# Optimization experiments

Measured on AMD Instinct MI355X. Metric: run time of the kernel, lower is better.

The kernel has to match this reference:

```python
import jax, jax.numpy as jnp
import numpy as np

N_ITERS = 5
STRICT_MAXIMA_BONUS = 10.0
MAX_SUBPIXEL_SHIFT = 0.6
DILATION_RADIUS = 1
EPS = 1e-7


def _dense_solve(x):
    """Per-voxel 3x3x3 quadratic-fit solve (Cramer's rule) on interior voxels.

    Returns full-size (zero-padded) sx, sy, ss, g.s, solved arrays.
    Axis convention: s = depth/scale (D), y = height (H), x = width (W).
    """
    c  = x[:, :, 1:-1, 1:-1, 1:-1]
    xp = x[:, :, 1:-1, 1:-1, 2:];   xm = x[:, :, 1:-1, 1:-1, :-2]
    yp = x[:, :, 1:-1, 2:, 1:-1];   ym = x[:, :, 1:-1, :-2, 1:-1]
    sp = x[:, :, 2:, 1:-1, 1:-1];   sm = x[:, :, :-2, 1:-1, 1:-1]
    xpyp = x[:, :, 1:-1, 2:, 2:];   xmyp = x[:, :, 1:-1, 2:, :-2]
    xpym = x[:, :, 1:-1, :-2, 2:];  xmym = x[:, :, 1:-1, :-2, :-2]
    xpsp = x[:, :, 2:, 1:-1, 2:];   xmsp = x[:, :, 2:, 1:-1, :-2]
    xpsm = x[:, :, :-2, 1:-1, 2:];  xmsm = x[:, :, :-2, 1:-1, :-2]
    ypsp = x[:, :, 2:, 2:, 1:-1];   ymsp = x[:, :, 2:, :-2, 1:-1]
    ypsm = x[:, :, :-2, 2:, 1:-1];  ymsm = x[:, :, :-2, :-2, 1:-1]
    gx = 0.5 * (xp - xm)
    gy = 0.5 * (yp - ym)
    gs = 0.5 * (sp - sm)
    dxx = xp - 2.0 * c + xm
    dyy = yp - 2.0 * c + ym
    dss = sp - 2.0 * c + sm
    dxy = 0.25 * (xpyp - xmyp - xpym + xmym)
    dxs = 0.25 * (xpsp - xmsp - xpsm + xmsm)
    dys = 0.25 * (ypsp - ymsp - ypsm + ymsm)
    cf00 = dyy * dss - dys * dys
    cf01 = dxy * dss - dys * dxs
    cf02 = dxy * dys - dyy * dxs
    det = dxx * cf00 - dxy * cf01 + dxs * cf02
    solved = jnp.abs(det) > EPS
    safe_det = jnp.where(solved, det, jnp.ones_like(det))
    r0, r1, r2 = -gx, -gy, -gs
    sx = (r0 * cf00 - dxy * (r1 * dss - dys * r2) + dxs * (r1 * dys - dyy * r2)) / safe_det
    sy = (dxx * (r1 * dss - dys * r2) - r0 * cf01 + dxs * (dxy * r2 - r1 * dxs)) / safe_det
    ss = (dxx * (dyy * r2 - r1 * dys) - dxy * (dxy * r2 - r1 * dxs) + r0 * cf02) / safe_det
    gds = gx * sx + gy * sy + gs * ss
    pad = ((0, 0), (0, 0), (1, 1), (1, 1), (1, 1))
    return (jnp.pad(sx, pad), jnp.pad(sy, pad), jnp.pad(ss, pad),
            jnp.pad(gds, pad), jnp.pad(solved, pad))


def reference(input, nms_mask):
    x = input
    B, C, D, H, W = x.shape
    dt = x.dtype
    HW = H * W
    DHW = D * HW
    r = DILATION_RADIUS

    sx_f, sy_f, ss_f, gds_f, sol_f = _dense_solve(x)
    sx_f = sx_f.reshape(-1); sy_f = sy_f.reshape(-1); ss_f = ss_f.reshape(-1)
    gds_f = gds_f.reshape(-1); sol_f = sol_f.reshape(-1)
    xf = x.reshape(-1)

    dg = jnp.arange(D, dtype=jnp.int32)[:, None, None]
    hg = jnp.arange(H, dtype=jnp.int32)[None, :, None]
    wg = jnp.arange(W, dtype=jnp.int32)[None, None, :]
    bcg = (jnp.arange(B * C, dtype=jnp.int32) * DHW).reshape(B, C, 1, 1, 1)

    zi = jnp.zeros((B, C, D, H, W), jnp.int32)
    dd, dh, dw = zi, zi, zi              # integer centre offsets (s, y, x)
    valid = nms_mask                      # only NMS maxima are tracked
    zf = jnp.zeros((B, C, D, H, W), dt)
    shift_x, shift_y, shift_s, gds_k = zf, zf, zf, zf

    for _ in range(N_ITERS):
        di = jnp.clip(dg + dd, 1, D - 2)
        hi = jnp.clip(hg + dh, 1, H - 2)
        wi = jnp.clip(wg + dw, 1, W - 2)
        flat = bcg + di * HW + hi * W + wi
        sx = sx_f[flat]; sy = sy_f[flat]; ss = ss_f[flat]
        gds = gds_f[flat]; sol = sol_f[flat]
        valid = valid & sol
        vf = valid.astype(dt)
        shift_x = sx * vf
        shift_y = sy * vf
        shift_s = ss * vf
        gds_k = gds * vf
        step_x = (jnp.sign(shift_x) * (jnp.abs(shift_x) > MAX_SUBPIXEL_SHIFT)).astype(jnp.int32)
        step_y = (jnp.sign(shift_y) * (jnp.abs(shift_y) > MAX_SUBPIXEL_SHIFT)).astype(jnp.int32)
        step_s = (jnp.sign(shift_s) * (jnp.abs(shift_s) > MAX_SUBPIXEL_SHIFT)).astype(jnp.int32)
        dw = dw + step_x; dh = dh + step_y; dd = dd + step_s
        # moving outside the dilated precompute region invalidates the keypoint
        valid = valid & (jnp.abs(dd) <= r) & (jnp.abs(dh) <= r) & (jnp.abs(dw) <= r)

    di = jnp.clip(dg + dd, 1, D - 2)
    hi = jnp.clip(hg + dh, 1, H - 2)
    wi = jnp.clip(wg + dw, 1, W - 2)
    flat = bcg + di * HW + hi * W + wi
    cur_val = xf[flat]

    refined = jnp.where(valid, cur_val + 0.5 * gds_k, x)
    y_max = jnp.where(nms_mask, refined + STRICT_MAXIMA_BONUS, x)

    fd = dg.astype(dt); fh = hg.astype(dt); fw = wg.astype(dt)
    cs = jnp.where(valid, (dg + dd).astype(dt) + shift_s, jnp.broadcast_to(fd, x.shape))
    cx = jnp.where(valid, (wg + dw).astype(dt) + shift_x, jnp.broadcast_to(fw, x.shape))
    cy = jnp.where(valid, (hg + dh).astype(dt) + shift_y, jnp.broadcast_to(fh, x.shape))
    coords_max = jnp.stack([cs, cx, cy], axis=2)  # (B,C,3,D,H,W): [scale, x, y]
    return coords_max, y_max


def setup_inputs() -> dict:
    key = jax.random.key(0)
    k1, k2 = jax.random.split(key)
    B, C, D, H, W = 2, 4, 6, 512, 512
    x = jax.random.normal(k1, (B, C, D, H, W), dtype=jnp.float32)
    m = jax.random.uniform(k2, (B, C, D, H, W)) < 0.001
    interior = jnp.zeros((B, C, D, H, W), dtype=bool).at[:, :, 1:-1, 1:-1, 1:-1].set(True)
    return {"input": x, "nms_mask": m & interior}
```

## Files before the change

kernel.cpp:

```cpp
#include <hip/hip_runtime.h>

#pragma clang fp contract(off)

constexpr int B_ = 2, C_ = 4, D_ = 6, H_ = 512, W_ = 512;
constexpr int HW_  = H_ * W_;
constexpr int DHW_ = D_ * HW_;
constexpr int BC_  = B_ * C_;
constexpr int TOT_ = BC_ * DHW_;

#define EPS_ 1e-7f
#define MAX_SHIFT_ 0.6f
#define BONUS_ 10.0f
#define N_ITERS_ 5

__device__ __forceinline__ void solve3(const float* __restrict__ p,
                                       float& sx, float& sy, float& ss,
                                       float& gds, bool& sol)
{
    #pragma clang fp contract(off)
    float c    = p[0];
    float xp   = p[1],          xm   = p[-1];
    float yp   = p[W_],         ym   = p[-W_];
    float spv  = p[HW_],        smv  = p[-HW_];
    float xpyp = p[W_ + 1],     xmyp = p[W_ - 1];
    float xpym = p[-W_ + 1],    xmym = p[-W_ - 1];
    float xpsp = p[HW_ + 1],    xmsp = p[HW_ - 1];
    float xpsm = p[-HW_ + 1],   xmsm = p[-HW_ - 1];
    float ypsp = p[HW_ + W_],   ymsp = p[HW_ - W_];
    float ypsm = p[-HW_ + W_],  ymsm = p[-HW_ - W_];

    float gx = 0.5f * (xp - xm);
    float gy = 0.5f * (yp - ym);
    float gs = 0.5f * (spv - smv);
    float dxx = xp - 2.0f * c + xm;
    float dyy = yp - 2.0f * c + ym;
    float dss = spv - 2.0f * c + smv;
    float dxy = 0.25f * (xpyp - xmyp - xpym + xmym);
    float dxs = 0.25f * (xpsp - xmsp - xpsm + xmsm);
    float dys = 0.25f * (ypsp - ymsp - ypsm + ymsm);

    float cf00 = dyy * dss - dys * dys;
    float cf01 = dxy * dss - dys * dxs;
    float cf02 = dxy * dys - dyy * dxs;
    float det  = dxx * cf00 - dxy * cf01 + dxs * cf02;
    sol = fabsf(det) > EPS_;
    float sd = sol ? det : 1.0f;
    float r0 = -gx, r1 = -gy, r2 = -gs;
    sx = (r0 * cf00 - dxy * (r1 * dss - dys * r2) + dxs * (r1 * dys - dyy * r2)) / sd;
    sy = (dxx * (r1 * dss - dys * r2) - r0 * cf01 + dxs * (dxy * r2 - r1 * dxs)) / sd;
    ss = (dxx * (dyy * r2 - r1 * dys) - dxy * (dxy * r2 - r1 * dxs) + r0 * cf02) / sd;
    gds = gx * sx + gy * sy + gs * ss;
}

__device__ __forceinline__ void walk_and_write(const float* __restrict__ x,
                                               float* __restrict__ out,
                                               int idx, float xc)
{
    #pragma clang fp contract(off)
    int w  = idx & (W_ - 1);
    int h  = (idx >> 9) & (H_ - 1);
    int t  = idx >> 18;
    int d  = t % D_;
    int bc = t / D_;
    int sp = idx - bc * DHW_;
    const float* xb = x + bc * DHW_;

    int dd = 0, dh = 0, dwo = 0;
    bool valid = true;
    float shx = 0.0f, shy = 0.0f, shs = 0.0f, gk = 0.0f;

    #pragma unroll 1
    for (int it = 0; it < N_ITERS_; ++it) {
        int di = min(max(d + dd, 1), D_ - 2);
        int hi = min(max(h + dh, 1), H_ - 2);
        int wi = min(max(w + dwo, 1), W_ - 2);
        const float* p = xb + di * HW_ + hi * W_ + wi;

        float sx, sy, ssv, gds; bool sol;
        solve3(p, sx, sy, ssv, gds, sol);

        valid = valid && sol;
        float vf = valid ? 1.0f : 0.0f;
        shx = sx * vf;
        shy = sy * vf;
        shs = ssv * vf;
        gk  = gds * vf;

        int stx = (shx > MAX_SHIFT_) ? 1 : ((shx < -MAX_SHIFT_) ? -1 : 0);
        int sty = (shy > MAX_SHIFT_) ? 1 : ((shy < -MAX_SHIFT_) ? -1 : 0);
        int sts = (shs > MAX_SHIFT_) ? 1 : ((shs < -MAX_SHIFT_) ? -1 : 0);
        dwo += stx;
        dh  += sty;
        dd  += sts;
        valid = valid && (abs(dd) <= 1) && (abs(dh) <= 1) && (abs(dwo) <= 1);
    }

    int di = min(max(d + dd, 1), D_ - 2);
    int hi = min(max(h + dh, 1), H_ - 2);
    int wi = min(max(w + dwo, 1), W_ - 2);
    float cur = xb[di * HW_ + hi * W_ + wi];

    float refined = valid ? (cur + 0.5f * gk) : xc;
    float yv = refined + BONUS_;
    float cs = valid ? ((float)(d + dd) + shs) : (float)d;
    float cx = valid ? ((float)(w + dwo) + shx) : (float)w;
    float cy = valid ? ((float)(h + dh) + shy) : (float)h;

    out[(bc * 3 + 0) * DHW_ + sp] = cs;
    out[(bc * 3 + 1) * DHW_ + sp] = cx;
    out[(bc * 3 + 2) * DHW_ + sp] = cy;
    out[BC_ * 3 * DHW_ + idx]     = yv;
}

__global__ __launch_bounds__(256)
void AdaptiveQuadInterp3d_kernel(const float4* __restrict__ x4,
                                 const int4*  __restrict__ m4,
                                 float* __restrict__ out)
{
    int tid  = blockIdx.x * 256 + threadIdx.x;
    int idx4 = tid << 2;

    int w  = idx4 & (W_ - 1);
    int h  = (idx4 >> 9) & (H_ - 1);
    int t  = idx4 >> 18;
    int d  = t % D_;
    int bc = t / D_;
    int sp = idx4 - bc * DHW_;

    float4 xv = x4[tid];
    int4   mv = m4[tid];

    *(float4*)(out + BC_ * 3 * DHW_ + idx4) = xv;

    float fd = (float)d, fh = (float)h;
    float4 csv = {fd, fd, fd, fd};
    float4 cxv = {(float)w, (float)(w + 1), (float)(w + 2), (float)(w + 3)};
    float4 cyv = {fh, fh, fh, fh};
    float* ob = out + (bc * 3) * DHW_ + sp;
    *(float4*)(ob)            = csv;
    *(float4*)(ob + DHW_)     = cxv;
    *(float4*)(ob + 2 * DHW_) = cyv;

    bool any_lane = (mv.x | mv.y | mv.z | mv.w) != 0;
    if (__ballot(any_lane) == 0ULL) return;

    const float* x = (const float*)x4;
    if (mv.x != 0) walk_and_write(x, out, idx4 + 0, xv.x);
    if (mv.y != 0) walk_and_write(x, out, idx4 + 1, xv.y);
    if (mv.z != 0) walk_and_write(x, out, idx4 + 2, xv.z);
    if (mv.w != 0) walk_and_write(x, out, idx4 + 3, xv.w);
}

extern "C" void kernel_launch(void* const* d_in, const int* in_sizes, int n_in,
                              void* d_out, int out_size, void* d_ws, size_t ws_size,
                              hipStream_t stream) {
    const float* x    = (const float*)d_in[0];
    const int*   mask = (const int*)d_in[1];
    float*       out  = (float*)d_out;

    int blocks = (TOT_ / 4) / 256;
    AdaptiveQuadInterp3d_kernel<<<blocks, 256, 0, stream>>>(
        (const float4*)x, (const int4*)mask, out);
}
```

Measured before the change: 283.0 us.

## Compact NMS seeds into a worklist and refine them in a separate sparse kernel

The single fused pass is split into a streaming kernel that writes the default outputs and appends masked voxel indices to a workspace list through wave-aggregated atomics. A second kernel then runs the quadratic-fit walk only on the listed seeds, so no wave has to serialise over up to four divergent walks. The walk now exits early on an invalid solve, on leaving the neighbourhood, or on convergence, and invalid seeds skip the coordinate writes. This adds two launches, a global atomic counter and a fixed list capacity that would silently drop seeds if the mask were denser than expected.

```diff
diff --git a/kernel.cpp b/kernel.cpp
--- a/kernel.cpp
+++ b/kernel.cpp
@@ -7,6 +7,7 @@
 constexpr int DHW_ = D_ * HW_;
 constexpr int BC_  = B_ * C_;
 constexpr int TOT_ = BC_ * DHW_;
+constexpr int CAP_ = 32768;
 
 #define EPS_ 1e-7f
 #define MAX_SHIFT_ 0.6f
@@ -52,9 +53,8 @@
     gds = gx * sx + gy * sy + gs * ss;
 }
 
-__device__ __forceinline__ void walk_and_write(const float* __restrict__ x,
-                                               float* __restrict__ out,
-                                               int idx, float xc)
+__device__ void walk_and_write(const float* __restrict__ x,
+                               float* __restrict__ out, int idx)
 {
     #pragma clang fp contract(off)
     int w  = idx & (W_ - 1);
@@ -64,6 +64,7 @@
     int bc = t / D_;
     int sp = idx - bc * DHW_;
     const float* xb = x + bc * DHW_;
+    float xc = x[idx];
 
     int dd = 0, dh = 0, dwo = 0;
     bool valid = true;
@@ -80,11 +81,9 @@
         solve3(p, sx, sy, ssv, gds, sol);
 
         valid = valid && sol;
-        float vf = valid ? 1.0f : 0.0f;
-        shx = sx * vf;
-        shy = sy * vf;
-        shs = ssv * vf;
-        gk  = gds * vf;
+        if (!valid) break;
+
+        shx = sx; shy = sy; shs = ssv; gk = gds;
 
         int stx = (shx > MAX_SHIFT_) ? 1 : ((shx < -MAX_SHIFT_) ? -1 : 0);
         int sty = (shy > MAX_SHIFT_) ? 1 : ((shy < -MAX_SHIFT_) ? -1 : 0);
@@ -92,30 +91,53 @@
         dwo += stx;
         dh  += sty;
         dd  += sts;
-        valid = valid && (abs(dd) <= 1) && (abs(dh) <= 1) && (abs(dwo) <= 1);
-    }
-
-    int di = min(max(d + dd, 1), D_ - 2);
-    int hi = min(max(h + dh, 1), H_ - 2);
-    int wi = min(max(w + dwo, 1), W_ - 2);
-    float cur = xb[di * HW_ + hi * W_ + wi];
-
-    float refined = valid ? (cur + 0.5f * gk) : xc;
-    float yv = refined + BONUS_;
-    float cs = valid ? ((float)(d + dd) + shs) : (float)d;
-    float cx = valid ? ((float)(w + dwo) + shx) : (float)w;
-    float cy = valid ? ((float)(h + dh) + shy) : (float)h;
-
-    out[(bc * 3 + 0) * DHW_ + sp] = cs;
-    out[(bc * 3 + 1) * DHW_ + sp] = cx;
-    out[(bc * 3 + 2) * DHW_ + sp] = cy;
-    out[BC_ * 3 * DHW_ + idx]     = yv;
+        valid = (abs(dd) <= 1) && (abs(dh) <= 1) && (abs(dwo) <= 1);
+        if (!valid) break;
+        if ((stx | sty | sts) == 0) break;
+    }
+
+    if (valid) {
+        int di = min(max(d + dd, 1), D_ - 2);
+        int hi = min(max(h + dh, 1), H_ - 2);
+        int wi = min(max(w + dwo, 1), W_ - 2);
+        float cur = xb[di * HW_ + hi * W_ + wi];
+        float refined = cur + 0.5f * gk;
+        out[(bc * 3 + 0) * DHW_ + sp] = (float)(d + dd)  + shs;
+        out[(bc * 3 + 1) * DHW_ + sp] = (float)(w + dwo) + shx;
+        out[(bc * 3 + 2) * DHW_ + sp] = (float)(h + dh)  + shy;
+        out[BC_ * 3 * DHW_ + idx]     = refined + BONUS_;
+    } else {
+        out[BC_ * 3 * DHW_ + idx]     = xc + BONUS_;
+    }
+}
+
+__global__ void zero_counter_kernel(unsigned int* __restrict__ counter)
+{
+    if (threadIdx.x == 0 && blockIdx.x == 0) counter[0] = 0u;
+}
+
+__device__ __forceinline__ void append_seed(int pred, int idx, int lane,
+                                            unsigned int* __restrict__ counter,
+                                            int* __restrict__ list)
+{
+    unsigned long long bal = __ballot(pred != 0);
+    if (bal != 0ULL) {
+        unsigned int base = 0;
+        if (lane == 0) base = atomicAdd(counter, (unsigned)__popcll(bal));
+        base = (unsigned)__shfl((int)base, 0, 64);
+        if (pred) {
+            unsigned int slot = base + (unsigned)__popcll(bal & ((1ULL << lane) - 1ULL));
+            if (slot < (unsigned)CAP_) list[slot] = idx;
+        }
+    }
 }
 
 __global__ __launch_bounds__(256)
-void AdaptiveQuadInterp3d_kernel(const float4* __restrict__ x4,
-                                 const int4*  __restrict__ m4,
-                                 float* __restrict__ out)
+void stream_kernel(const float4* __restrict__ x4,
+                   const int4*  __restrict__ m4,
+                   float* __restrict__ out,
+                   unsigned int* __restrict__ counter,
+                   int* __restrict__ list)
 {
     int tid  = blockIdx.x * 256 + threadIdx.x;
     int idx4 = tid << 2;
@@ -141,14 +163,61 @@
     *(float4*)(ob + DHW_)     = cxv;
     *(float4*)(ob + 2 * DHW_) = cyv;
 
+    int lane = threadIdx.x & 63;
+    append_seed(mv.x, idx4 + 0, lane, counter, list);
+    append_seed(mv.y, idx4 + 1, lane, counter, list);
+    append_seed(mv.z, idx4 + 2, lane, counter, list);
+    append_seed(mv.w, idx4 + 3, lane, counter, list);
+}
+
+__global__ __launch_bounds__(256)
+void sparse_kernel(const float* __restrict__ x,
+                   float* __restrict__ out,
+                   const unsigned int* __restrict__ counter,
+                   const int* __restrict__ list)
+{
+    unsigned int n = counter[0];
+    if (n > (unsigned)CAP_) n = CAP_;
+    unsigned int tid = blockIdx.x * 256 + threadIdx.x;
+    if (tid >= n) return;
+    walk_and_write(x, out, list[tid]);
+}
+
+__global__ __launch_bounds__(256)
+void fused_kernel(const float4* __restrict__ x4,
+                  const int4*  __restrict__ m4,
+                  float* __restrict__ out)
+{
+    int tid  = blockIdx.x * 256 + threadIdx.x;
+    int idx4 = tid << 2;
+    int w  = idx4 & (W_ - 1);
+    int h  = (idx4 >> 9) & (H_ - 1);
+    int t  = idx4 >> 18;
+    int d  = t % D_;
+    int bc = t / D_;
+    int sp = idx4 - bc * DHW_;
+
+    float4 xv = x4[tid];
+    int4   mv = m4[tid];
+
+    *(float4*)(out + BC_ * 3 * DHW_ + idx4) = xv;
+    float fd = (float)d, fh = (float)h;
+    float4 csv = {fd, fd, fd, fd};
+    float4 cxv = {(float)w, (float)(w + 1), (float)(w + 2), (float)(w + 3)};
+    float4 cyv = {fh, fh, fh, fh};
+    float* ob = out + (bc * 3) * DHW_ + sp;
+    *(float4*)(ob)            = csv;
+    *(float4*)(ob + DHW_)     = cxv;
+    *(float4*)(ob + 2 * DHW_) = cyv;
+
     bool any_lane = (mv.x | mv.y | mv.z | mv.w) != 0;
     if (__ballot(any_lane) == 0ULL) return;
 
     const float* x = (const float*)x4;
-    if (mv.x != 0) walk_and_write(x, out, idx4 + 0, xv.x);
-    if (mv.y != 0) walk_and_write(x, out, idx4 + 1, xv.y);
-    if (mv.z != 0) walk_and_write(x, out, idx4 + 2, xv.z);
-    if (mv.w != 0) walk_and_write(x, out, idx4 + 3, xv.w);
+    if (mv.x != 0) walk_and_write(x, out, idx4 + 0);
+    if (mv.y != 0) walk_and_write(x, out, idx4 + 1);
+    if (mv.z != 0) walk_and_write(x, out, idx4 + 2);
+    if (mv.w != 0) walk_and_write(x, out, idx4 + 3);
 }
 
 extern "C" void kernel_launch(void* const* d_in, const int* in_sizes, int n_in,
@@ -158,7 +227,20 @@
     const int*   mask = (const int*)d_in[1];
     float*       out  = (float*)d_out;
 
-    int blocks = (TOT_ / 4) / 256;
-    AdaptiveQuadInterp3d_kernel<<<blocks, 256, 0, stream>>>(
-        (const float4*)x, (const int4*)mask, out);
-}
+    size_t need = 256 + (size_t)CAP_ * sizeof(int);
+    if (ws_size >= need) {
+        unsigned int* counter = (unsigned int*)d_ws;
+        int*          list    = (int*)((char*)d_ws + 256);
+
+        zero_counter_kernel<<<1, 64, 0, stream>>>(counter);
+        int blocksA = (TOT_ / 4) / 256;
+        stream_kernel<<<blocksA, 256, 0, stream>>>(
+            (const float4*)x, (const int4*)mask, out, counter, list);
+        int blocksB = CAP_ / 256;
+        sparse_kernel<<<blocksB, 256, 0, stream>>>(x, out, counter, list);
+    } else {
+        int blocks = (TOT_ / 4) / 256;
+        fused_kernel<<<blocks, 256, 0, stream>>>(
+            (const float4*)x, (const int4*)mask, out);
+    }
+}
```

Measured after the change: 322.2 us. +13.9%, slower.
